# Performance work log

Measured on AMD Instinct MI355X. Metric: run time of the kernel, lower is better.

The kernel has to match this reference:

```python
import jax, jax.numpy as jnp
import numpy as np

T, D, N, H = 2032, 1408, 16, 88  # K == N (MHA vision attention)
BLOCK_SIZE = 128
ROPE_THETA = 10000.0


def _apply_rope_interleaved(x_tnh, freqs_cis):
    # x_tnh: [T, N, H]; freqs_cis: [T, H//2, 2] with (..., 0)=cos, (..., 1)=sin.
    cos = freqs_cis[:, None, :, 0]  # [T, 1, H//2]
    sin = freqs_cis[:, None, :, 1]
    x1 = x_tnh[..., 0::2]
    x2 = x_tnh[..., 1::2]
    # interleaved rotation: pairs (even, odd) rotated by angle theta_t
    rot = jnp.stack([x1 * cos - x2 * sin, x1 * sin + x2 * cos], axis=-1)
    return rot.reshape(x_tnh.shape)


def setup_inputs() -> dict:
    key = jax.random.key(0)
    ks = jax.random.split(key, 10)
    s = 0.02
    x = jax.random.normal(ks[0], (T, D), dtype=jnp.float32)
    # precomputed rotary cos/sin table (interleaved ordering)
    pos = jnp.arange(T, dtype=jnp.float32)
    inv_freq = ROPE_THETA ** (-jnp.arange(0, H, 2, dtype=jnp.float32) / H)  # [H//2]
    ang = pos[:, None] * inv_freq[None, :]                                  # [T, H//2]
    freqs_cis = jnp.stack([jnp.cos(ang), jnp.sin(ang)], axis=-1)            # [T, H//2, 2]
    Wq = jax.random.normal(ks[1], (D, N, H), dtype=jnp.float32) * s
    Wk = jax.random.normal(ks[2], (D, N, H), dtype=jnp.float32) * s
    Wv = jax.random.normal(ks[3], (D, N, H), dtype=jnp.float32) * s
    Wo = jax.random.normal(ks[4], (N, H, D), dtype=jnp.float32) * s
    bq = jax.random.normal(ks[5], (N, H), dtype=jnp.float32) * s
    bk = jax.random.normal(ks[6], (N, H), dtype=jnp.float32) * s
    bv = jax.random.normal(ks[7], (N, H), dtype=jnp.float32) * s
    bo = jax.random.normal(ks[8], (D,), dtype=jnp.float32) * s
    return {"x": x, "freqs_cis": freqs_cis, "Wq": Wq, "bq": bq, "Wk": Wk,
            "bk": bk, "Wv": Wv, "bv": bv, "Wo": Wo, "bo": bo}


def reference(x, freqs_cis, Wq, bq, Wk, bk, Wv, bv, Wo, bo):
    t, d = x.shape
    n, h = bq.shape
    sm_scale = h ** -0.5
    # fused QKV projections + bias + RoPE (q, k only)
    q = jnp.einsum('td,dnh->tnh', x, Wq) + bq[None]
    q = _apply_rope_interleaved(q, freqs_cis)
    k = jnp.einsum('td,dkh->tkh', x, Wk) + bk[None]
    k = _apply_rope_interleaved(k, freqs_cis)
    v = jnp.einsum('td,dkh->tkh', x, Wv) + bv[None]
    # pad T up to a multiple of BLOCK_SIZE, as the flash-attention call requires
    pad_len = (BLOCK_SIZE - t % BLOCK_SIZE) % BLOCK_SIZE
    qp = jnp.pad(q, ((0, pad_len), (0, 0), (0, 0)))
    kp = jnp.pad(k, ((0, pad_len), (0, 0), (0, 0)))
    vp = jnp.pad(v, ((0, pad_len), (0, 0), (0, 0)))
    # [N, Tp, H]
    qh = jnp.transpose(qp, (1, 0, 2))
    kh = jnp.transpose(kp, (1, 0, 2))
    vh = jnp.transpose(vp, (1, 0, 2))
    # segment ids: 0 for valid tokens, 1 for padding; attention only within equal ids
    seg = jnp.concatenate([jnp.zeros((t,), jnp.int32), jnp.ones((pad_len,), jnp.int32)])
    mask = seg[:, None] == seg[None, :]  # [Tp, Tp]
    scores = jnp.einsum('nth,nsh->nts', qh, kh) * sm_scale
    scores = jnp.where(mask[None], scores, jnp.finfo(scores.dtype).min)
    probs = jax.nn.softmax(scores, axis=-1)
    out = jnp.einsum('nts,nsh->nth', probs, vh)        # [N, Tp, H]
    out = jnp.transpose(out, (1, 0, 2))[:t]            # [T, N, H]
    o = jnp.einsum('tnh,nhd->td', out, Wo) + bo
    return o
```

## Files before the change

### kernel.cpp

```cpp
#include <hip/hip_runtime.h>
#include <hip/hip_bf16.h>
#include <stdint.h>
#include <stddef.h>

typedef __bf16 bf16_t;
typedef __bf16 bf16x8 __attribute__((ext_vector_type(8)));
typedef __bf16 bf16x4 __attribute__((ext_vector_type(4)));
typedef float  f32x4  __attribute__((ext_vector_type(4)));

#define T_SEQ 2032
#define T_PAD 2048
#define DM    1408
#define NHEAD 16
#define HD    88
#define HPQ   96
#define HPK   128
#define HPV   96
#define SM_SCALE 0.10660035817780521f

__device__ __forceinline__ void gload_lds16(const bf16_t* g, bf16_t* l) {
  __builtin_amdgcn_global_load_lds(
      (__attribute__((address_space(1))) void*)(g),
      (__attribute__((address_space(3))) void*)(l), 16, 0, 0);
}

__global__ void k_convert_x(const float* __restrict__ x, bf16_t* __restrict__ Xb) {
  int idx = blockIdx.x * 256 + threadIdx.x;
  const int total = T_PAD * DM / 4;
  if (idx >= total) return;
  int base = idx * 4;
  int t = base / DM;
  float4 v;
  if (t < T_SEQ) v = *(const float4*)(x + base);
  else           v = make_float4(0.f, 0.f, 0.f, 0.f);
  bf16x4 o;
  o[0] = (bf16_t)v.x; o[1] = (bf16_t)v.y; o[2] = (bf16_t)v.z; o[3] = (bf16_t)v.w;
  *(bf16x4*)(Xb + base) = o;
}

__device__ __forceinline__ void transpose_body(const float* __restrict__ src,
                                               bf16_t* __restrict__ dst,
                                               int R, int C, int blk) {
  __shared__ float tile[32][33];
  const int tiles_c = C >> 5;
  const int tr = blk / tiles_c;
  const int tc = blk % tiles_c;
  const int lane = threadIdx.x & 31;
  const int row  = threadIdx.x >> 5;
#pragma unroll
  for (int i = 0; i < 32; i += 8)
    tile[row + i][lane] = src[(size_t)(tr * 32 + row + i) * C + tc * 32 + lane];
  __syncthreads();
#pragma unroll
  for (int i = 0; i < 32; i += 8)
    dst[(size_t)(tc * 32 + row + i) * R + tr * 32 + lane] = (bf16_t)tile[lane][row + i];
}

__global__ void k_transpose3(const float* __restrict__ Wq, const float* __restrict__ Wk,
                             const float* __restrict__ Wv, bf16_t* __restrict__ dst) {
  const int which = blockIdx.x / 1936;
  const int b = blockIdx.x % 1936;
  const float* src = (which == 0) ? Wq : (which == 1) ? Wk : Wv;
  transpose_body(src, dst + (size_t)which * DM * DM, DM, DM, b);
}

__global__ void k_transpose1(const float* __restrict__ src, bf16_t* __restrict__ dst) {
  transpose_body(src, dst, DM, DM, blockIdx.x);
}

__global__ void k_bias(const float* __restrict__ bq, const float* __restrict__ bk,
                       const float* __restrict__ bv, float* __restrict__ bias) {
  int i = blockIdx.x * 256 + threadIdx.x;
  if (i >= 3 * DM) return;
  bias[i] = (i < DM) ? bq[i] : ((i < 2 * DM) ? bk[i - DM] : bv[i - 2 * DM]);
}

__global__ void k_rope(bf16_t* __restrict__ Q, bf16_t* __restrict__ K,
                       const float* __restrict__ freqs) {
  int idx = blockIdx.x * 256 + threadIdx.x;
  const int TOT = 2 * NHEAD * T_SEQ * 44;
  if (idx >= TOT) return;
  int i = idx % 44;
  int t = (idx / 44) % T_SEQ;
  int n = (idx / (44 * T_SEQ)) % NHEAD;
  int which = idx / (44 * T_SEQ * NHEAD);
  bf16_t* P = which ? (K + ((size_t)n * T_PAD + t) * HPK + 2 * i)
                    : (Q + ((size_t)n * T_PAD + t) * HPQ + 2 * i);
  float c = freqs[t * 88 + 2 * i];
  float s = freqs[t * 88 + 2 * i + 1];
  float x1 = (float)P[0], x2 = (float)P[1];
  float sc = which ? 1.0f : SM_SCALE;
  P[0] = (bf16_t)((x1 * c - x2 * s) * sc);
  P[1] = (bf16_t)((x1 * s + x2 * c) * sc);
}

__device__ __forceinline__ void gemm_main_1408(
    const bf16_t* __restrict__ A, const bf16_t* __restrict__ Bt,
    bf16_t* As, bf16_t* Bs, int m0, int n0, f32x4 acc[4][4]) {
  const int tid = threadIdx.x;
  const int w = tid >> 6, lane = tid & 63;
  const int l15 = lane & 15, lg = lane >> 4;
  const int b0 = w * 2048 + lane * 16;
  const int r0 = b0 >> 6, k0 = (b0 & 63) >> 1;
  const int b1 = b0 + 1024;
  const int r1 = b1 >> 6, k1 = (b1 & 63) >> 1;
  const int wr = w >> 1, wc = w & 1;
  const size_t aoff0 = (size_t)(m0 + r0) * DM + k0;
  const size_t aoff1 = (size_t)(m0 + r1) * DM + k1;
  const size_t boff0 = (size_t)(n0 + r0) * DM + k0;
  const size_t boff1 = (size_t)(n0 + r1) * DM + k1;
  for (int kt = 0; kt < 44; ++kt) {
    const int ko = kt * 32;
    gload_lds16(A + aoff0 + ko, As + w * 1024);
    gload_lds16(A + aoff1 + ko, As + w * 1024 + 512);
    gload_lds16(Bt + boff0 + ko, Bs + w * 1024);
    gload_lds16(Bt + boff1 + ko, Bs + w * 1024 + 512);
    __syncthreads();
    bf16x8 av[4], bv[4];
#pragma unroll
    for (int m = 0; m < 4; ++m)
      av[m] = *(const bf16x8*)(As + (wr * 64 + m * 16 + l15) * 32 + lg * 8);
#pragma unroll
    for (int n = 0; n < 4; ++n)
      bv[n] = *(const bf16x8*)(Bs + (wc * 64 + n * 16 + l15) * 32 + lg * 8);
#pragma unroll
    for (int m = 0; m < 4; ++m)
#pragma unroll
      for (int n = 0; n < 4; ++n)
        acc[m][n] = __builtin_amdgcn_mfma_f32_16x16x32_bf16(av[m], bv[n], acc[m][n], 0, 0, 0);
    __syncthreads();
  }
}

__global__ __launch_bounds__(256, 2) void k_gemm_qkv(
    const bf16_t* __restrict__ A, const bf16_t* __restrict__ Bt,
    const float* __restrict__ bias,
    bf16_t* __restrict__ Qh, bf16_t* __restrict__ Kh, bf16_t* __restrict__ Vt) {
  __shared__ bf16_t As[128 * 32];
  __shared__ bf16_t Bs[128 * 32];
  const int mt = blockIdx.x / 33, nt = blockIdx.x % 33;
  f32x4 acc[4][4];
#pragma unroll
  for (int m = 0; m < 4; ++m)
#pragma unroll
    for (int n = 0; n < 4; ++n) acc[m][n] = (f32x4){0.f, 0.f, 0.f, 0.f};
  gemm_main_1408(A, Bt, As, Bs, mt * 128, nt * 128, acc);
  const int tid = threadIdx.x, w = tid >> 6, lane = tid & 63;
  const int l15 = lane & 15, lg = lane >> 4;
  const int wr = w >> 1, wc = w & 1;
  const int cb = nt * 128 + wc * 64, rb = mt * 128 + wr * 64;
#pragma unroll
  for (int n = 0; n < 4; ++n) {
    const int col = cb + n * 16 + l15;
    const float bv = bias[col];
    const int seg = (col >= 2 * DM) ? 2 : ((col >= DM) ? 1 : 0);
    const int cc = col - seg * DM;
    const int hn = cc / 88;
    const int hh = cc - hn * 88;
#pragma unroll
    for (int m = 0; m < 4; ++m) {
      const int tb = rb + m * 16 + lg * 4;
      if (seg == 2) {
        bf16x4 vv;
#pragma unroll
        for (int r = 0; r < 4; ++r) vv[r] = (bf16_t)(acc[m][n][r] + bv);
        *(bf16x4*)(Vt + ((size_t)hn * HPV + hh) * T_PAD + tb) = vv;
      } else if (seg == 0) {
#pragma unroll
        for (int r = 0; r < 4; ++r)
          Qh[((size_t)hn * T_PAD + tb + r) * HPQ + hh] = (bf16_t)(acc[m][n][r] + bv);
      } else {
#pragma unroll
        for (int r = 0; r < 4; ++r)
          Kh[((size_t)hn * T_PAD + tb + r) * HPK + hh] = (bf16_t)(acc[m][n][r] + bv);
      }
    }
  }
}

__global__ __launch_bounds__(256, 2) void k_gemm_out64(
    const bf16_t* __restrict__ A, const bf16_t* __restrict__ Bt,
    const float* __restrict__ bo, float* __restrict__ out) {
  __shared__ bf16_t Sm[6144];
  const int mt = blockIdx.x / 11, nt = blockIdx.x % 11;
  const int m0 = mt * 64, n0 = nt * 128;
  const int tid = threadIdx.x, w = tid >> 6, lane = tid & 63;
  const int l15 = lane & 15, lg = lane >> 4;
  const bf16_t* srcp[3];
  size_t srco[3];
  int dste[3];
#pragma unroll
  for (int p = 0; p < 3; ++p) {
    const int off = w * 3072 + p * 1024;
    const int o = off + lane * 16;
    dste[p] = off >> 1;
    if (off < 4096) {
      int r = o >> 6, k = (o & 63) >> 1;
      srcp[p] = A; srco[p] = (size_t)(m0 + r) * DM + k;
    } else {
      int ob = o - 4096;
      int r = ob >> 6, k = (ob & 63) >> 1;
      srcp[p] = Bt; srco[p] = (size_t)(n0 + r) * DM + k;
    }
  }
  f32x4 acc[4][2];
#pragma unroll
  for (int m = 0; m < 4; ++m)
#pragma unroll
    for (int n = 0; n < 2; ++n) acc[m][n] = (f32x4){0.f, 0.f, 0.f, 0.f};
  for (int kt = 0; kt < 44; ++kt) {
    const int ko = kt * 32;
#pragma unroll
    for (int p = 0; p < 3; ++p)
      gload_lds16(srcp[p] + srco[p] + ko, Sm + dste[p]);
    __syncthreads();
    bf16x8 av[4], bv2[2];
#pragma unroll
    for (int m = 0; m < 4; ++m)
      av[m] = *(const bf16x8*)(Sm + (m * 16 + l15) * 32 + lg * 8);
#pragma unroll
    for (int n = 0; n < 2; ++n)
      bv2[n] = *(const bf16x8*)(Sm + 2048 + (w * 32 + n * 16 + l15) * 32 + lg * 8);
#pragma unroll
    for (int m = 0; m < 4; ++m)
#pragma unroll
      for (int n = 0; n < 2; ++n)
        acc[m][n] = __builtin_amdgcn_mfma_f32_16x16x32_bf16(av[m], bv2[n], acc[m][n], 0, 0, 0);
    __syncthreads();
  }
  const int cb = n0 + w * 32;
#pragma unroll
  for (int n = 0; n < 2; ++n) {
    const int col = cb + n * 16 + l15;
    const float bv = bo[col];
#pragma unroll
    for (int m = 0; m < 4; ++m) {
#pragma unroll
      for (int r = 0; r < 4; ++r) {
        const int t = m0 + m * 16 + lg * 4 + r;
        if (t < T_SEQ) out[(size_t)t * DM + col] = acc[m][n][r] + bv;
      }
    }
  }
}

__global__ __launch_bounds__(256, 2) void k_attn(
    const bf16_t* __restrict__ Qh, const bf16_t* __restrict__ Kh,
    const bf16_t* __restrict__ Vt, bf16_t* __restrict__ Ob) {
  __shared__ bf16_t Ks[128 * 128];
  __shared__ bf16_t Vs[HPV * 128];
  __shared__ bf16_t Ps[4][16 * 128];
  const int tid = threadIdx.x;
  const int w = tid >> 6, lane = tid & 63;
  const int l15 = lane & 15, lg = lane >> 4;
  const int swz = l15 & 7;
  const int head = blockIdx.x >> 5;
  const int qt = blockIdx.x & 31;
  const bf16_t* Qn = Qh + (size_t)head * T_PAD * HPQ;
  const bf16_t* Kn = Kh + (size_t)head * T_PAD * HPK;
  const bf16_t* Vn = Vt + (size_t)head * HPV * T_PAD;
  const int q0 = qt * 64 + w * 16;

  bf16x8 qf[3];
#pragma unroll
  for (int kh = 0; kh < 3; ++kh)
    qf[kh] = *(const bf16x8*)(Qn + (size_t)(q0 + l15) * HPQ + kh * 32 + lg * 8);

  f32x4 oacc[6];
#pragma unroll
  for (int j = 0; j < 6; ++j) oacc[j] = (f32x4){0.f, 0.f, 0.f, 0.f};
  float mrow[4] = {-1e30f, -1e30f, -1e30f, -1e30f};
  float lrow[4] = {0.f, 0.f, 0.f, 0.f};

  int ko_e[8];
#pragma unroll
  for (int p = 0; p < 8; ++p) {
    int o = (w * 8 + p) * 1024 + lane * 16;
    int row = o >> 8, ch = (o >> 4) & 15;
    ko_e[p] = row * HPK + ((ch ^ (row & 7)) << 3);
  }
  int vo_e[6];
#pragma unroll
  for (int p = 0; p < 6; ++p) {
    int o = (w * 6 + p) * 1024 + lane * 16;
    int row = o >> 8, ch = (o >> 4) & 15;
    vo_e[p] = row * T_PAD + ((ch ^ (row & 7)) << 3);
  }

  for (int kvt = 0; kvt < 16; ++kvt) {
    const int s0 = kvt * 128;
#pragma unroll
    for (int p = 0; p < 8; ++p)
      gload_lds16(Kn + (size_t)s0 * HPK + ko_e[p], Ks + (w * 8 + p) * 512);
#pragma unroll
    for (int p = 0; p < 6; ++p)
      gload_lds16(Vn + s0 + vo_e[p], Vs + (w * 6 + p) * 512);
    __syncthreads();

    f32x4 sf[8];
#pragma unroll
    for (int ss = 0; ss < 8; ++ss) {
      const int rowK = ss * 16 + l15;
      f32x4 s = {0.f, 0.f, 0.f, 0.f};
#pragma unroll
      for (int kh = 0; kh < 3; ++kh) {
        bf16x8 kf = *(const bf16x8*)(Ks + rowK * 128 + (((kh * 4 + lg) ^ swz) << 3));
        s = __builtin_amdgcn_mfma_f32_16x16x32_bf16(qf[kh], kf, s, 0, 0, 0);
      }
      if (s0 + rowK >= T_SEQ) s = (f32x4){-1e30f, -1e30f, -1e30f, -1e30f};
      sf[ss] = s;
    }
    float tm[4];
#pragma unroll
    for (int r = 0; r < 4; ++r) {
      float v = sf[0][r];
#pragma unroll
      for (int ss = 1; ss < 8; ++ss) v = fmaxf(v, sf[ss][r]);
      tm[r] = v;
    }
#pragma unroll
    for (int d = 1; d < 16; d <<= 1)
#pragma unroll
      for (int r = 0; r < 4; ++r) tm[r] = fmaxf(tm[r], __shfl_xor(tm[r], d, 16));
    float sc[4];
#pragma unroll
    for (int r = 0; r < 4; ++r) {
      float mn = fmaxf(mrow[r], tm[r]);
      sc[r] = __expf(mrow[r] - mn);
      mrow[r] = mn;
    }
    float rs[4] = {0.f, 0.f, 0.f, 0.f};
#pragma unroll
    for (int ss = 0; ss < 8; ++ss)
#pragma unroll
      for (int r = 0; r < 4; ++r) {
        float p = __expf(sf[ss][r] - mrow[r]);
        sf[ss][r] = p;
        rs[r] += p;
      }
#pragma unroll
    for (int d = 1; d < 16; d <<= 1)
#pragma unroll
      for (int r = 0; r < 4; ++r) rs[r] += __shfl_xor(rs[r], d, 16);
#pragma unroll
    for (int r = 0; r < 4; ++r) lrow[r] = lrow[r] * sc[r] + rs[r];
#pragma unroll
    for (int j = 0; j < 6; ++j)
#pragma unroll
      for (int r = 0; r < 4; ++r) oacc[j][r] *= sc[r];
#pragma unroll
    for (int ss = 0; ss < 8; ++ss)
#pragma unroll
      for (int r = 0; r < 4; ++r) {
        const int row = lg * 4 + r;
        Ps[w][row * 128 + (((2 * ss + (l15 >> 3)) ^ (row & 7)) << 3) + (l15 & 7)] =
            (bf16_t)sf[ss][r];
      }
    bf16x8 pa[4];
#pragma unroll
    for (int ks = 0; ks < 4; ++ks)
      pa[ks] = *(const bf16x8*)(&Ps[w][l15 * 128 + (((ks * 4 + lg) ^ swz) << 3)]);
#pragma unroll
    for (int j = 0; j < 6; ++j)
#pragma unroll
      for (int ks = 0; ks < 4; ++ks) {
        bf16x8 vf = *(const bf16x8*)(Vs + (j * 16 + l15) * 128 + (((ks * 4 + lg) ^ swz) << 3));
        oacc[j] = __builtin_amdgcn_mfma_f32_16x16x32_bf16(pa[ks], vf, oacc[j], 0, 0, 0);
      }
    __syncthreads();
  }
#pragma unroll
  for (int j = 0; j < 6; ++j) {
    const int h = j * 16 + l15;
    if (h < HD) {
#pragma unroll
      for (int r = 0; r < 4; ++r) {
        const int t = q0 + lg * 4 + r;
        if (t < T_SEQ)
          Ob[(size_t)t * DM + head * HD + h] = (bf16_t)(oacc[j][r] / lrow[r]);
      }
    }
  }
}

extern "C" void kernel_launch(void* const* d_in, const int* in_sizes, int n_in,
                              void* d_out, int out_size, void* d_ws, size_t ws_size,
                              hipStream_t stream) {
  (void)in_sizes; (void)n_in; (void)out_size; (void)ws_size;
  const float* x     = (const float*)d_in[0];
  const float* freqs = (const float*)d_in[1];
  const float* Wq    = (const float*)d_in[2];
  const float* bq    = (const float*)d_in[3];
  const float* Wk    = (const float*)d_in[4];
  const float* bk    = (const float*)d_in[5];
  const float* Wv    = (const float*)d_in[6];
  const float* bv    = (const float*)d_in[7];
  const float* Wo    = (const float*)d_in[8];
  const float* bo    = (const float*)d_in[9];
  float* out = (float*)d_out;
  char* ws = (char*)d_ws;

  bf16_t* Xb   = (bf16_t*)(ws);
  bf16_t* Wt   = (bf16_t*)(ws + 5767168);
  float*  bias = (float*) (ws + 17661952);
  bf16_t* Qh   = (bf16_t*)(ws + 17678848);
  bf16_t* Kh   = (bf16_t*)(ws + 23970304);
  bf16_t* Vt   = (bf16_t*)(ws + 32358912);
  bf16_t* Ob   = Xb;
  bf16_t* Wot  = Wt;

  hipMemsetAsync(Qh, 0, 14680064, stream);

  k_convert_x<<<(T_PAD * DM / 4 + 255) / 256, 256, 0, stream>>>(x, Xb);
  k_transpose3<<<3 * 1936, 256, 0, stream>>>(Wq, Wk, Wv, Wt);
  k_bias<<<17, 256, 0, stream>>>(bq, bk, bv, bias);

  k_gemm_qkv<<<16 * 33, 256, 0, stream>>>(Xb, Wt, bias, Qh, Kh, Vt);
  k_rope<<<2 * NHEAD * T_SEQ * 44 / 256, 256, 0, stream>>>(Qh, Kh, freqs);

  k_transpose1<<<1936, 256, 0, stream>>>(Wo, Wot);

  k_attn<<<NHEAD * 32, 256, 0, stream>>>(Qh, Kh, Vt, Ob);
  k_gemm_out64<<<32 * 11, 256, 0, stream>>>(Ob, Wot, bo, out);
}
```

Measured before the change: 255.6 us.

## Fuse RoPE into QKV GEMM epilogue and pipeline attention with smaller KV tiles

```diff
diff --git a/kernel.cpp b/kernel.cpp
--- a/kernel.cpp
+++ b/kernel.cpp
@@ -16,6 +16,8 @@
 #define HPQ   96
 #define HPK   128
 #define HPV   96
+#define KVB   64
+#define NT    (T_PAD / KVB)
 #define SM_SCALE 0.10660035817780521f
 
 __device__ __forceinline__ void gload_lds16(const bf16_t* g, bf16_t* l) {
@@ -73,25 +75,6 @@
   int i = blockIdx.x * 256 + threadIdx.x;
   if (i >= 3 * DM) return;
   bias[i] = (i < DM) ? bq[i] : ((i < 2 * DM) ? bk[i - DM] : bv[i - 2 * DM]);
-}
-
-__global__ void k_rope(bf16_t* __restrict__ Q, bf16_t* __restrict__ K,
-                       const float* __restrict__ freqs) {
-  int idx = blockIdx.x * 256 + threadIdx.x;
-  const int TOT = 2 * NHEAD * T_SEQ * 44;
-  if (idx >= TOT) return;
-  int i = idx % 44;
-  int t = (idx / 44) % T_SEQ;
-  int n = (idx / (44 * T_SEQ)) % NHEAD;
-  int which = idx / (44 * T_SEQ * NHEAD);
-  bf16_t* P = which ? (K + ((size_t)n * T_PAD + t) * HPK + 2 * i)
-                    : (Q + ((size_t)n * T_PAD + t) * HPQ + 2 * i);
-  float c = freqs[t * 88 + 2 * i];
-  float s = freqs[t * 88 + 2 * i + 1];
-  float x1 = (float)P[0], x2 = (float)P[1];
-  float sc = which ? 1.0f : SM_SCALE;
-  P[0] = (bf16_t)((x1 * c - x2 * s) * sc);
-  P[1] = (bf16_t)((x1 * s + x2 * c) * sc);
 }
 
 __device__ __forceinline__ void gemm_main_1408(
@@ -134,11 +117,13 @@
 
 __global__ __launch_bounds__(256, 2) void k_gemm_qkv(
     const bf16_t* __restrict__ A, const bf16_t* __restrict__ Bt,
-    const float* __restrict__ bias,
+    const float* __restrict__ bias, const float* __restrict__ freqs,
     bf16_t* __restrict__ Qh, bf16_t* __restrict__ Kh, bf16_t* __restrict__ Vt) {
   __shared__ bf16_t As[128 * 32];
   __shared__ bf16_t Bs[128 * 32];
-  const int mt = blockIdx.x / 33, nt = blockIdx.x % 33;
+  const int bid = blockIdx.x;
+  const int sbid = (bid & 7) * 66 + (bid >> 3);
+  const int mt = sbid / 33, nt = sbid % 33;
   f32x4 acc[4][4];
 #pragma unroll
   for (int m = 0; m < 4; ++m)
@@ -157,6 +142,8 @@
     const int cc = col - seg * DM;
     const int hn = cc / 88;
     const int hh = cc - hn * 88;
+    const int hbase = hh & ~1;
+    const bool odd = hh & 1;
 #pragma unroll
     for (int m = 0; m < 4; ++m) {
       const int tb = rb + m * 16 + lg * 4;
@@ -165,14 +152,23 @@
 #pragma unroll
         for (int r = 0; r < 4; ++r) vv[r] = (bf16_t)(acc[m][n][r] + bv);
         *(bf16x4*)(Vt + ((size_t)hn * HPV + hh) * T_PAD + tb) = vv;
-      } else if (seg == 0) {
-#pragma unroll
-        for (int r = 0; r < 4; ++r)
-          Qh[((size_t)hn * T_PAD + tb + r) * HPQ + hh] = (bf16_t)(acc[m][n][r] + bv);
       } else {
 #pragma unroll
-        for (int r = 0; r < 4; ++r)
-          Kh[((size_t)hn * T_PAD + tb + r) * HPK + hh] = (bf16_t)(acc[m][n][r] + bv);
+        for (int r = 0; r < 4; ++r) {
+          const int t = tb + r;
+          const float v = acc[m][n][r] + bv;
+          const float p = __shfl_xor(v, 1);
+          const int tc2 = (t < T_SEQ) ? t : 0;
+          const float c = freqs[tc2 * 88 + hbase];
+          const float s = freqs[tc2 * 88 + hbase + 1];
+          const float x1 = odd ? p : v;
+          const float x2 = odd ? v : p;
+          const float ro = odd ? (x1 * s + x2 * c) : (x1 * c - x2 * s);
+          if (seg == 0)
+            Qh[((size_t)hn * T_PAD + t) * HPQ + hh] = (bf16_t)(ro * SM_SCALE);
+          else
+            Kh[((size_t)hn * T_PAD + t) * HPK + hh] = (bf16_t)ro;
+        }
       }
     }
   }
@@ -182,7 +178,9 @@
     const bf16_t* __restrict__ A, const bf16_t* __restrict__ Bt,
     const float* __restrict__ bo, float* __restrict__ out) {
   __shared__ bf16_t Sm[6144];
-  const int mt = blockIdx.x / 11, nt = blockIdx.x % 11;
+  const int bid = blockIdx.x;
+  const int sbid = (bid & 7) * 44 + (bid >> 3);
+  const int mt = sbid / 11, nt = sbid % 11;
   const int m0 = mt * 64, n0 = nt * 128;
   const int tid = threadIdx.x, w = tid >> 6, lane = tid & 63;
   const int l15 = lane & 15, lg = lane >> 4;
@@ -244,18 +242,20 @@
   }
 }
 
-__global__ __launch_bounds__(256, 2) void k_attn(
+__global__ __launch_bounds__(256, 3) void k_attn(
     const bf16_t* __restrict__ Qh, const bf16_t* __restrict__ Kh,
     const bf16_t* __restrict__ Vt, bf16_t* __restrict__ Ob) {
-  __shared__ bf16_t Ks[128 * 128];
-  __shared__ bf16_t Vs[HPV * 128];
-  __shared__ bf16_t Ps[4][16 * 128];
+  __shared__ bf16_t Ks[2][KVB * 128];
+  __shared__ bf16_t Vs[HPV * KVB];
+  __shared__ bf16_t Ps[4][16 * 72];
   const int tid = threadIdx.x;
   const int w = tid >> 6, lane = tid & 63;
   const int l15 = lane & 15, lg = lane >> 4;
   const int swz = l15 & 7;
-  const int head = blockIdx.x >> 5;
-  const int qt = blockIdx.x & 31;
+  const int bid = blockIdx.x;
+  const int sbid = (bid & 7) * 64 + (bid >> 3);
+  const int head = sbid >> 5;
+  const int qt = sbid & 31;
   const bf16_t* Qn = Qh + (size_t)head * T_PAD * HPQ;
   const bf16_t* Kn = Kh + (size_t)head * T_PAD * HPK;
   const bf16_t* Vn = Vt + (size_t)head * HPV * T_PAD;
@@ -270,54 +270,61 @@
 #pragma unroll
   for (int j = 0; j < 6; ++j) oacc[j] = (f32x4){0.f, 0.f, 0.f, 0.f};
   float mrow[4] = {-1e30f, -1e30f, -1e30f, -1e30f};
-  float lrow[4] = {0.f, 0.f, 0.f, 0.f};
-
-  int ko_e[8];
-#pragma unroll
-  for (int p = 0; p < 8; ++p) {
-    int o = (w * 8 + p) * 1024 + lane * 16;
+  float lrowp[4] = {0.f, 0.f, 0.f, 0.f};
+
+  int kro[4], kco[4];
+#pragma unroll
+  for (int p = 0; p < 4; ++p) {
+    int o = (w * 4 + p) * 1024 + lane * 16;
     int row = o >> 8, ch = (o >> 4) & 15;
-    ko_e[p] = row * HPK + ((ch ^ (row & 7)) << 3);
-  }
-  int vo_e[6];
-#pragma unroll
-  for (int p = 0; p < 6; ++p) {
-    int o = (w * 6 + p) * 1024 + lane * 16;
-    int row = o >> 8, ch = (o >> 4) & 15;
-    vo_e[p] = row * T_PAD + ((ch ^ (row & 7)) << 3);
-  }
-
-  for (int kvt = 0; kvt < 16; ++kvt) {
-    const int s0 = kvt * 128;
-#pragma unroll
-    for (int p = 0; p < 8; ++p)
-      gload_lds16(Kn + (size_t)s0 * HPK + ko_e[p], Ks + (w * 8 + p) * 512);
-#pragma unroll
-    for (int p = 0; p < 6; ++p)
-      gload_lds16(Vn + s0 + vo_e[p], Vs + (w * 6 + p) * 512);
-    __syncthreads();
-
-    f32x4 sf[8];
-#pragma unroll
-    for (int ss = 0; ss < 8; ++ss) {
+    kro[p] = row; kco[p] = (ch ^ (row & 7)) << 3;
+  }
+  int vro[3], vco[3];
+#pragma unroll
+  for (int p = 0; p < 3; ++p) {
+    int o = (w * 3 + p) * 1024 + lane * 16;
+    int row = o >> 7, ch = (o >> 4) & 7;
+    vro[p] = row; vco[p] = (ch ^ (row & 7)) << 3;
+  }
+
+#pragma unroll
+  for (int p = 0; p < 4; ++p)
+    gload_lds16(Kn + (size_t)kro[p] * HPK + kco[p], &Ks[0][(w * 4 + p) * 512]);
+#pragma unroll
+  for (int p = 0; p < 3; ++p)
+    gload_lds16(Vn + (size_t)vro[p] * T_PAD + vco[p], &Vs[(w * 3 + p) * 512]);
+
+  for (int kvt = 0; kvt < NT; ++kvt) {
+    const int s0 = kvt * KVB;
+    const int cur = kvt & 1;
+    const int nxt = (kvt + 1 < NT) ? kvt + 1 : 0;
+#pragma unroll
+    for (int p = 0; p < 4; ++p)
+      gload_lds16(Kn + (size_t)(nxt * KVB + kro[p]) * HPK + kco[p],
+                  &Ks[cur ^ 1][(w * 4 + p) * 512]);
+    asm volatile("s_waitcnt vmcnt(4)" ::: "memory");
+    __builtin_amdgcn_s_barrier();
+
+    const bf16_t* Kc = Ks[cur];
+    f32x4 sf[4];
+    __builtin_amdgcn_s_setprio(1);
+#pragma unroll
+    for (int ss = 0; ss < 4; ++ss) {
       const int rowK = ss * 16 + l15;
       f32x4 s = {0.f, 0.f, 0.f, 0.f};
 #pragma unroll
       for (int kh = 0; kh < 3; ++kh) {
-        bf16x8 kf = *(const bf16x8*)(Ks + rowK * 128 + (((kh * 4 + lg) ^ swz) << 3));
+        bf16x8 kf = *(const bf16x8*)(Kc + rowK * 128 + (((kh * 4 + lg) ^ swz) << 3));
         s = __builtin_amdgcn_mfma_f32_16x16x32_bf16(qf[kh], kf, s, 0, 0, 0);
       }
       if (s0 + rowK >= T_SEQ) s = (f32x4){-1e30f, -1e30f, -1e30f, -1e30f};
       sf[ss] = s;
     }
+    __builtin_amdgcn_s_setprio(0);
     float tm[4];
 #pragma unroll
-    for (int r = 0; r < 4; ++r) {
-      float v = sf[0][r];
-#pragma unroll
-      for (int ss = 1; ss < 8; ++ss) v = fmaxf(v, sf[ss][r]);
-      tm[r] = v;
-    }
+    for (int r = 0; r < 4; ++r)
+      tm[r] = fmaxf(fmaxf(sf[0][r], sf[1][r]), fmaxf(sf[2][r], sf[3][r]));
 #pragma unroll
     for (int d = 1; d < 16; d <<= 1)
 #pragma unroll
@@ -329,46 +336,52 @@
       sc[r] = __expf(mrow[r] - mn);
       mrow[r] = mn;
     }
-    float rs[4] = {0.f, 0.f, 0.f, 0.f};
-#pragma unroll
-    for (int ss = 0; ss < 8; ++ss)
-#pragma unroll
-      for (int r = 0; r < 4; ++r) {
+#pragma unroll
+    for (int r = 0; r < 4; ++r) {
+      float rs = 0.f;
+#pragma unroll
+      for (int ss = 0; ss < 4; ++ss) {
         float p = __expf(sf[ss][r] - mrow[r]);
         sf[ss][r] = p;
-        rs[r] += p;
-      }
-#pragma unroll
-    for (int d = 1; d < 16; d <<= 1)
-#pragma unroll
-      for (int r = 0; r < 4; ++r) rs[r] += __shfl_xor(rs[r], d, 16);
-#pragma unroll
-    for (int r = 0; r < 4; ++r) lrow[r] = lrow[r] * sc[r] + rs[r];
+        rs += p;
+      }
+      lrowp[r] = lrowp[r] * sc[r] + rs;
+    }
 #pragma unroll
     for (int j = 0; j < 6; ++j)
 #pragma unroll
       for (int r = 0; r < 4; ++r) oacc[j][r] *= sc[r];
 #pragma unroll
-    for (int ss = 0; ss < 8; ++ss)
-#pragma unroll
-      for (int r = 0; r < 4; ++r) {
-        const int row = lg * 4 + r;
-        Ps[w][row * 128 + (((2 * ss + (l15 >> 3)) ^ (row & 7)) << 3) + (l15 & 7)] =
-            (bf16_t)sf[ss][r];
-      }
-    bf16x8 pa[4];
-#pragma unroll
-    for (int ks = 0; ks < 4; ++ks)
-      pa[ks] = *(const bf16x8*)(&Ps[w][l15 * 128 + (((ks * 4 + lg) ^ swz) << 3)]);
+    for (int ss = 0; ss < 4; ++ss)
+#pragma unroll
+      for (int r = 0; r < 4; ++r)
+        Ps[w][(lg * 4 + r) * 72 + ss * 16 + l15] = (bf16_t)sf[ss][r];
+    bf16x8 pa[2];
+#pragma unroll
+    for (int ks = 0; ks < 2; ++ks)
+      pa[ks] = *(const bf16x8*)(&Ps[w][l15 * 72 + ks * 32 + lg * 8]);
+    __builtin_amdgcn_s_setprio(1);
 #pragma unroll
     for (int j = 0; j < 6; ++j)
 #pragma unroll
-      for (int ks = 0; ks < 4; ++ks) {
-        bf16x8 vf = *(const bf16x8*)(Vs + (j * 16 + l15) * 128 + (((ks * 4 + lg) ^ swz) << 3));
+      for (int ks = 0; ks < 2; ++ks) {
+        bf16x8 vf = *(const bf16x8*)(Vs + (j * 16 + l15) * KVB + (((ks * 4 + lg) ^ swz) << 3));
         oacc[j] = __builtin_amdgcn_mfma_f32_16x16x32_bf16(pa[ks], vf, oacc[j], 0, 0, 0);
       }
-    __syncthreads();
-  }
+    __builtin_amdgcn_s_setprio(0);
+    __builtin_amdgcn_s_barrier();
+#pragma unroll
+    for (int p = 0; p < 3; ++p)
+      gload_lds16(Vn + (size_t)vro[p] * T_PAD + nxt * KVB + vco[p],
+                  &Vs[(w * 3 + p) * 512]);
+  }
+  asm volatile("s_waitcnt vmcnt(0)" ::: "memory");
+
+#pragma unroll
+  for (int d = 1; d < 16; d <<= 1)
+#pragma unroll
+    for (int r = 0; r < 4; ++r) lrowp[r] += __shfl_xor(lrowp[r], d, 16);
+
 #pragma unroll
   for (int j = 0; j < 6; ++j) {
     const int h = j * 16 + l15;
@@ -377,7 +390,7 @@
       for (int r = 0; r < 4; ++r) {
         const int t = q0 + lg * 4 + r;
         if (t < T_SEQ)
-          Ob[(size_t)t * DM + head * HD + h] = (bf16_t)(oacc[j][r] / lrow[r]);
+          Ob[(size_t)t * DM + head * HD + h] = (bf16_t)(oacc[j][r] / lrowp[r]);
       }
     }
   }
@@ -415,8 +428,7 @@
   k_transpose3<<<3 * 1936, 256, 0, stream>>>(Wq, Wk, Wv, Wt);
   k_bias<<<17, 256, 0, stream>>>(bq, bk, bv, bias);
 
-  k_gemm_qkv<<<16 * 33, 256, 0, stream>>>(Xb, Wt, bias, Qh, Kh, Vt);
-  k_rope<<<2 * NHEAD * T_SEQ * 44 / 256, 256, 0, stream>>>(Qh, Kh, freqs);
+  k_gemm_qkv<<<16 * 33, 256, 0, stream>>>(Xb, Wt, bias, freqs, Qh, Kh, Vt);
 
   k_transpose1<<<1936, 256, 0, stream>>>(Wo, Wot);
 
```

Result: no change. 256.5 us (+0.3%).
